# Kernel tuning notes

Hardware: AMD Instinct MI355X
Metric: run time of the kernel (lower is better)

## Reference

```python
import jax, jax.numpy as jnp
import numpy as np

B, D, C = 256, 512, 100000
U_M, L_M = 0.8, 0.45
U_A, L_A = 110.0, 10.0
LAMBDA_G = 35.0
SCALE = 64.0


def setup_inputs() -> dict:
    key = jax.random.key(0)
    k1, k2, k3, k4 = jax.random.split(key, 4)
    x = jax.random.normal(k1, (B, D), dtype=jnp.float32)
    # per-sample feature magnitudes in [l_a, u_a]
    x_norm = L_A + jax.random.uniform(k2, (B, 1), dtype=jnp.float32) * (U_A - L_A)
    labels = jax.random.randint(k3, (B,), 0, C)
    weight = jax.random.normal(k4, (C, D), dtype=jnp.float32)
    return {"x": x, "x_norm": x_norm, "labels": labels, "weight": weight}


def reference(x, x_norm, labels, weight):
    # adaptive margin m(a) = slope * (a - l_a) + l_m, per sample [B,1]
    ada_margin = (U_M - L_M) / (U_A - L_A) * (x_norm - L_A) + L_M
    cos_m = jnp.cos(ada_margin)
    sin_m = jnp.sin(ada_margin)

    xn = x / jnp.linalg.norm(x, axis=-1, keepdims=True)          # [B,D]
    wn = weight / jnp.linalg.norm(weight, axis=-1, keepdims=True)  # [C,D]
    cos_theta = jnp.clip(jnp.einsum('bd,cd->bc', xn, wn), -1.0, 1.0)  # [B,C]
    sin_theta = jnp.sqrt(1.0 - cos_theta * cos_theta)
    cos_theta_m = cos_theta * cos_m - sin_theta * sin_m
    # easy_margin=True: only apply margin where cos_theta > 0
    cos_theta_m = jnp.where(cos_theta > 0, cos_theta_m, cos_theta)

    one_hot = jax.nn.one_hot(labels, C, dtype=cos_theta.dtype)   # [B,C]
    logits = SCALE * (one_hot * cos_theta_m + (1.0 - one_hot) * cos_theta)

    # cross-entropy with mean reduction
    tgt = jnp.take_along_axis(logits, labels[:, None], axis=1)[:, 0]
    ce = jnp.mean(jax.nn.logsumexp(logits, axis=1) - tgt)

    # MagFace G-loss: mean(a / u_a^2 + 1/a)
    loss_g = jnp.mean(x_norm / (U_A * U_A) + 1.0 / x_norm)
    return ce + LAMBDA_G * loss_g
```

## Files before the change

### kernel.cpp

```cpp
#include <hip/hip_runtime.h>
#include <hip/hip_bf16.h>

#define BB 256
#define DD 512
#define CNUM 100000
#define CPAD 100096
#define BN2 64
#define NCH 1564
#define NPART NCH

typedef __attribute__((ext_vector_type(8))) short bf16x8;
typedef __attribute__((ext_vector_type(4))) float f32x4;

__device__ __forceinline__ unsigned short f2bf(float f) {
  union { float f; unsigned int u; } v; v.f = f;
  unsigned int u = v.u;
  unsigned int r = u + 0x7FFFu + ((u >> 16) & 1u);
  return (unsigned short)(r >> 16);
}

__global__ void k_prep_x(const float* __restrict__ x, const float* __restrict__ xnrm,
                         unsigned short* __restrict__ xt, float* __restrict__ cm,
                         float* __restrict__ sm) {
  int b = blockIdx.x;
  int lane = threadIdx.x;
  const float4* xr = (const float4*)(x + (size_t)b * DD);
  float4 v0 = xr[lane * 2];
  float4 v1 = xr[lane * 2 + 1];
  float ss = v0.x * v0.x + v0.y * v0.y + v0.z * v0.z + v0.w * v0.w +
             v1.x * v1.x + v1.y * v1.y + v1.z * v1.z + v1.w * v1.w;
#pragma unroll
  for (int msk = 1; msk < 64; msk <<= 1) ss += __shfl_xor(ss, msk, 64);
  float inv = rsqrtf(ss);
  unsigned int p0 = (unsigned int)f2bf(v0.x * inv) | ((unsigned int)f2bf(v0.y * inv) << 16);
  unsigned int p1 = (unsigned int)f2bf(v0.z * inv) | ((unsigned int)f2bf(v0.w * inv) << 16);
  unsigned int p2 = (unsigned int)f2bf(v1.x * inv) | ((unsigned int)f2bf(v1.y * inv) << 16);
  unsigned int p3 = (unsigned int)f2bf(v1.z * inv) | ((unsigned int)f2bf(v1.w * inv) << 16);
  size_t idx = ((size_t)(lane >> 2) * BB + b) * 32 + (lane & 3) * 8;
  *(uint4*)(xt + idx) = make_uint4(p0, p1, p2, p3);
  if (lane == 0) {
    float a = xnrm[b];
    float marg = 0.0035f * (a - 10.0f) + 0.45f;
    cm[b] = cosf(marg);
    sm[b] = sinf(marg);
  }
}

__global__ __launch_bounds__(256) void k_gemm(
    const unsigned short* __restrict__ xt, const float* __restrict__ w,
    const int* __restrict__ labels, const float* __restrict__ cmv,
    const float* __restrict__ smv, float2* __restrict__ part, float* __restrict__ tgt) {
  __shared__ short Ws[2][BN2 * 64];
  __shared__ float sInvW[BN2];
  __shared__ int sLab[BB];
  __shared__ float sCm[BB], sSm[BB];

  int tid = threadIdx.x, wave = tid >> 6, lane = tid & 63;
  int cbase = blockIdx.x * BN2;
  int cfrag = lane & 15, g = lane >> 4;

  sLab[tid] = labels[tid];
  sCm[tid] = cmv[tid];
  sSm[tid] = smv[tid];

  int wrow = tid >> 2, wseg = tid & 3;
  int wr_c = cbase + wrow;
  if (wr_c >= CNUM) wr_c = 0;
  const float* wptr = w + (size_t)wr_c * DD + wseg * 16;
  float ssacc = 0.0f;
  int wsw0 = wrow * 64 + ((wseg * 16) ^ ((wrow & 7) << 3));
  int wsw1 = wrow * 64 + ((wseg * 16 + 8) ^ ((wrow & 7) << 3));

  const unsigned short* xb = xt + (size_t)(wave * 64 + cfrag) * 32 + g * 8;

  f32x4 acc[4][4];
#pragma unroll
  for (int m = 0; m < 4; ++m)
#pragma unroll
    for (int n = 0; n < 4; ++n) acc[m][n] = (f32x4){0.f, 0.f, 0.f, 0.f};

  f32x4 wv[4];

#define LOAD_W(T)                                                              \
  _Pragma("unroll") for (int j = 0; j < 4; ++j)                                \
      wv[j] = *(const f32x4*)(wptr + (T) * 64 + j * 4);

#define PACK_W(B)                                                              \
  {                                                                            \
    f32x4 a = wv[0], b = wv[1], c = wv[2], d = wv[3];                          \
    ssacc += a[0]*a[0] + a[1]*a[1] + a[2]*a[2] + a[3]*a[3] +                   \
             b[0]*b[0] + b[1]*b[1] + b[2]*b[2] + b[3]*b[3] +                   \
             c[0]*c[0] + c[1]*c[1] + c[2]*c[2] + c[3]*c[3] +                   \
             d[0]*d[0] + d[1]*d[1] + d[2]*d[2] + d[3]*d[3];                    \
    unsigned int q0 = (unsigned int)f2bf(a[0]) | ((unsigned int)f2bf(a[1]) << 16); \
    unsigned int q1 = (unsigned int)f2bf(a[2]) | ((unsigned int)f2bf(a[3]) << 16); \
    unsigned int q2 = (unsigned int)f2bf(b[0]) | ((unsigned int)f2bf(b[1]) << 16); \
    unsigned int q3 = (unsigned int)f2bf(b[2]) | ((unsigned int)f2bf(b[3]) << 16); \
    unsigned int q4 = (unsigned int)f2bf(c[0]) | ((unsigned int)f2bf(c[1]) << 16); \
    unsigned int q5 = (unsigned int)f2bf(c[2]) | ((unsigned int)f2bf(c[3]) << 16); \
    unsigned int q6 = (unsigned int)f2bf(d[0]) | ((unsigned int)f2bf(d[1]) << 16); \
    unsigned int q7 = (unsigned int)f2bf(d[2]) | ((unsigned int)f2bf(d[3]) << 16); \
    *(uint4*)&Ws[B][wsw0] = make_uint4(q0, q1, q2, q3);                        \
    *(uint4*)&Ws[B][wsw1] = make_uint4(q4, q5, q6, q7);                        \
  }

  LOAD_W(0);
  PACK_W(0);
  LOAD_W(1);
  __syncthreads();

#pragma unroll
  for (int kc = 0; kc < 8; ++kc) {
    const int p = kc & 1;
    bf16x8 af0[4], af1[4];
#pragma unroll
    for (int m = 0; m < 4; ++m) {
      af0[m] = *(const bf16x8*)(xb + ((size_t)(2 * kc) * BB + m * 16) * 32);
      af1[m] = *(const bf16x8*)(xb + ((size_t)(2 * kc + 1) * BB + m * 16) * 32);
    }
    if (kc < 7) {
      PACK_W(p ^ 1);
      if (kc < 6) LOAD_W(kc + 2);
    }
#pragma unroll
    for (int ks = 0; ks < 2; ++ks) {
      int krd = ks * 32 + g * 8;
      int swz = (lane & 7) << 3;
      bf16x8 bfr[4];
#pragma unroll
      for (int n = 0; n < 4; ++n) {
        int rb = n * 16 + cfrag;
        bfr[n] = *(const bf16x8*)&Ws[p][rb * 64 + (krd ^ swz)];
      }
#pragma unroll
      for (int m = 0; m < 4; ++m)
#pragma unroll
        for (int n = 0; n < 4; ++n)
          acc[m][n] = __builtin_amdgcn_mfma_f32_16x16x32_bf16(
              ks ? af1[m] : af0[m], bfr[n], acc[m][n], 0, 0, 0);
    }
    __syncthreads();
  }
#undef LOAD_W
#undef PACK_W

  ssacc += __shfl_xor(ssacc, 1, 64);
  ssacc += __shfl_xor(ssacc, 2, 64);
  if (wseg == 0) sInvW[wrow] = rsqrtf(ssacc);
  __syncthreads();

  float invc[4];
#pragma unroll
  for (int n = 0; n < 4; ++n) {
    int col = cbase + n * 16 + cfrag;
    invc[n] = (col < CNUM) ? sInvW[n * 16 + cfrag] : 0.0f;
  }
#pragma unroll
  for (int m = 0; m < 4; ++m) {
#pragma unroll
    for (int r = 0; r < 4; ++r) {
      int row = wave * 64 + m * 16 + g * 4 + r;
      int lab = sLab[row];
      float cmr = sCm[row], smr = sSm[row];
      float lg[4];
      float vmax = -1e30f;
#pragma unroll
      for (int n = 0; n < 4; ++n) {
        int col = cbase + n * 16 + cfrag;
        float cv = acc[m][n][r] * invc[n];
        cv = fminf(1.0f, fmaxf(-1.0f, cv));
        float logit;
        if (col == lab) {
          float st = sqrtf(fmaxf(0.0f, 1.0f - cv * cv));
          float cm2 = cv * cmr - st * smr;
          logit = 64.0f * (cv > 0.0f ? cm2 : cv);
          tgt[row] = logit;
        } else {
          logit = 64.0f * cv;
        }
        if (col >= CNUM) logit = -1e30f;
        lg[n] = logit;
        vmax = fmaxf(vmax, logit);
      }
#pragma unroll
      for (int msk = 1; msk < 16; msk <<= 1) vmax = fmaxf(vmax, __shfl_xor(vmax, msk, 64));
      float s = 0.0f;
#pragma unroll
      for (int n = 0; n < 4; ++n) s += __expf(lg[n] - vmax);
#pragma unroll
      for (int msk = 1; msk < 16; msk <<= 1) s += __shfl_xor(s, msk, 64);
      if (cfrag == 0) part[(size_t)row * NPART + blockIdx.x] = make_float2(vmax, s);
    }
  }
}

__global__ void k_merge(const float2* __restrict__ part, const float* __restrict__ tgt,
                        float* __restrict__ ce) {
  int b = blockIdx.x, t = threadIdx.x;
  float m = -1e30f, s = 0.0f;
  for (int i = t; i < NPART; i += 256) {
    float2 p = part[(size_t)b * NPART + i];
    float nm = fmaxf(m, p.x);
    s = s * __expf(m - nm) + p.y * __expf(p.x - nm);
    m = nm;
  }
  __shared__ float smx[256], ssm[256];
  smx[t] = m;
  ssm[t] = s;
  __syncthreads();
  for (int off = 128; off > 0; off >>= 1) {
    if (t < off) {
      float m2 = smx[t + off], s2 = ssm[t + off];
      float nm = fmaxf(smx[t], m2);
      ssm[t] = ssm[t] * __expf(smx[t] - nm) + s2 * __expf(m2 - nm);
      smx[t] = nm;
    }
    __syncthreads();
  }
  if (t == 0) ce[b] = smx[0] + logf(ssm[0]) - tgt[b];
}

__global__ void k_final(const float* __restrict__ ce, const float* __restrict__ xnrm,
                        float* __restrict__ out) {
  int t = threadIdx.x;
  float cv = ce[t];
  float a = xnrm[t];
  float gv = a * (1.0f / (110.0f * 110.0f)) + 1.0f / a;
  __shared__ float s1[256], s2[256];
  s1[t] = cv;
  s2[t] = gv;
  __syncthreads();
  for (int off = 128; off > 0; off >>= 1) {
    if (t < off) {
      s1[t] += s1[t + off];
      s2[t] += s2[t + off];
    }
    __syncthreads();
  }
  if (t == 0) out[0] = s1[0] * (1.0f / 256.0f) + 35.0f * s2[0] * (1.0f / 256.0f);
}

extern "C" void kernel_launch(void* const* d_in, const int* in_sizes, int n_in,
                              void* d_out, int out_size, void* d_ws, size_t ws_size,
                              hipStream_t stream) {
  const float* x = (const float*)d_in[0];
  const float* xnrm = (const float*)d_in[1];
  const int* labels = (const int*)d_in[2];
  const float* w = (const float*)d_in[3];

  char* ws = (char*)d_ws;
  unsigned short* XT = (unsigned short*)ws;
  size_t off = (size_t)BB * DD * 2;
  float* CM = (float*)(ws + off);  off += 1024;
  float* SM = (float*)(ws + off);  off += 1024;
  float* TGT = (float*)(ws + off); off += 1024;
  float* CE = (float*)(ws + off);  off += 1024;
  float2* PART = (float2*)(ws + off);

  k_prep_x<<<BB, 64, 0, stream>>>(x, xnrm, XT, CM, SM);
  k_gemm<<<NCH, 256, 0, stream>>>(XT, w, labels, CM, SM, PART, TGT);
  k_merge<<<BB, 256, 0, stream>>>(PART, TGT, CE);
  k_final<<<1, 256, 0, stream>>>(CE, xnrm, (float*)d_out);
}
```

Before: 97.47 us.

## Widen GEMM tile to 128 classes per block with 8 waves and register-prefetched A fragments

Each block now covers 128 weight rows with 512 threads arranged as a 4x2 wave grid, halving the grid size while keeping the per-wave 64x64 tile. X fragments are double-buffered in registers and loaded one step ahead. The __syncthreads calls are replaced by lgkmcnt waits plus s_barrier, with compiler fences around the weight loads. The aim is to reuse the X tile across more classes per block and overlap global loads with MFMA work, at the cost of more registers per thread and lower occupancy.

```diff
diff --git a/kernel.cpp b/kernel.cpp
--- a/kernel.cpp
+++ b/kernel.cpp
@@ -5,9 +5,8 @@
 #define DD 512
 #define CNUM 100000
 #define CPAD 100096
-#define BN2 64
-#define NCH 1564
-#define NPART NCH
+#define NCHUNK 782
+#define NPART (NCHUNK * 2)
 
 typedef __attribute__((ext_vector_type(8))) short bf16x8;
 typedef __attribute__((ext_vector_type(4))) float f32x4;
@@ -46,22 +45,25 @@
   }
 }
 
-__global__ __launch_bounds__(256) void k_gemm(
+__global__ __launch_bounds__(512) void k_gemm(
     const unsigned short* __restrict__ xt, const float* __restrict__ w,
     const int* __restrict__ labels, const float* __restrict__ cmv,
     const float* __restrict__ smv, float2* __restrict__ part, float* __restrict__ tgt) {
-  __shared__ short Ws[2][BN2 * 64];
-  __shared__ float sInvW[BN2];
+  __shared__ short Ws[2][128 * 64];
+  __shared__ float sInvW[128];
   __shared__ int sLab[BB];
   __shared__ float sCm[BB], sSm[BB];
 
   int tid = threadIdx.x, wave = tid >> 6, lane = tid & 63;
-  int cbase = blockIdx.x * BN2;
+  int wm = wave >> 1, wq = wave & 1;
+  int cbase = blockIdx.x * 128;
   int cfrag = lane & 15, g = lane >> 4;
 
-  sLab[tid] = labels[tid];
-  sCm[tid] = cmv[tid];
-  sSm[tid] = smv[tid];
+  if (tid < BB) {
+    sLab[tid] = labels[tid];
+    sCm[tid] = cmv[tid];
+    sSm[tid] = smv[tid];
+  }
 
   int wrow = tid >> 2, wseg = tid & 3;
   int wr_c = cbase + wrow;
@@ -71,7 +73,7 @@
   int wsw0 = wrow * 64 + ((wseg * 16) ^ ((wrow & 7) << 3));
   int wsw1 = wrow * 64 + ((wseg * 16 + 8) ^ ((wrow & 7) << 3));
 
-  const unsigned short* xb = xt + (size_t)(wave * 64 + cfrag) * 32 + g * 8;
+  const unsigned short* xtb = xt + (size_t)(wm * 64 + cfrag) * 32 + g * 8;
 
   f32x4 acc[4][4];
 #pragma unroll
@@ -79,15 +81,21 @@
 #pragma unroll
     for (int n = 0; n < 4; ++n) acc[m][n] = (f32x4){0.f, 0.f, 0.f, 0.f};
 
-  f32x4 wv[4];
-
-#define LOAD_W(T)                                                              \
+  f32x4 wv[2][4];
+  bf16x8 af[2][2][4];
+
+#define LOAD_W(T, S)                                                           \
   _Pragma("unroll") for (int j = 0; j < 4; ++j)                                \
-      wv[j] = *(const f32x4*)(wptr + (T) * 64 + j * 4);
-
-#define PACK_W(B)                                                              \
+      wv[S][j] = *(const f32x4*)(wptr + (T) * 64 + j * 4);
+
+#define LOAD_AF(T, S)                                                          \
+  _Pragma("unroll") for (int h = 0; h < 2; ++h)                                \
+  _Pragma("unroll") for (int m = 0; m < 4; ++m)                                \
+      af[S][h][m] = *(const bf16x8*)(xtb + (size_t)(2 * (T) + h) * (BB * 32) + m * 512);
+
+#define PACK_W(S, B)                                                           \
   {                                                                            \
-    f32x4 a = wv[0], b = wv[1], c = wv[2], d = wv[3];                          \
+    f32x4 a = wv[S][0], b = wv[S][1], c = wv[S][2], d = wv[S][3];              \
     ssacc += a[0]*a[0] + a[1]*a[1] + a[2]*a[2] + a[3]*a[3] +                   \
              b[0]*b[0] + b[1]*b[1] + b[2]*b[2] + b[3]*b[3] +                   \
              c[0]*c[0] + c[1]*c[1] + c[2]*c[2] + c[3]*c[3] +                   \
@@ -104,69 +112,72 @@
     *(uint4*)&Ws[B][wsw1] = make_uint4(q4, q5, q6, q7);                        \
   }
 
-  LOAD_W(0);
-  PACK_W(0);
-  LOAD_W(1);
-  __syncthreads();
+#define COMPUTE(T)                                                             \
+  _Pragma("unroll") for (int ks = 0; ks < 2; ++ks) {                           \
+    int krd = ks * 32 + g * 8;                                                 \
+    int swz = (lane & 7) << 3;                                                 \
+    bf16x8 bfr[4];                                                             \
+    _Pragma("unroll") for (int n = 0; n < 4; ++n) {                            \
+      int rb = wq * 64 + n * 16 + cfrag;                                       \
+      bfr[n] = *(const bf16x8*)&Ws[(T) & 1][rb * 64 + (krd ^ swz)];            \
+    }                                                                          \
+    _Pragma("unroll") for (int m = 0; m < 4; ++m)                              \
+      _Pragma("unroll") for (int n = 0; n < 4; ++n)                            \
+        acc[m][n] = __builtin_amdgcn_mfma_f32_16x16x32_bf16(                   \
+            af[(T) & 1][ks][m], bfr[n], acc[m][n], 0, 0, 0);                   \
+  }
+
+#define FENCE asm volatile("" ::: "memory")
+#define BARRIER asm volatile("s_waitcnt lgkmcnt(0)\n\ts_barrier" ::: "memory")
+
+  LOAD_W(0, 0);
+  LOAD_W(1, 1);
+  FENCE;
+  PACK_W(0, 0);
+  LOAD_AF(0, 0);
+  BARRIER;
 
 #pragma unroll
   for (int kc = 0; kc < 8; ++kc) {
-    const int p = kc & 1;
-    bf16x8 af0[4], af1[4];
-#pragma unroll
-    for (int m = 0; m < 4; ++m) {
-      af0[m] = *(const bf16x8*)(xb + ((size_t)(2 * kc) * BB + m * 16) * 32);
-      af1[m] = *(const bf16x8*)(xb + ((size_t)(2 * kc + 1) * BB + m * 16) * 32);
-    }
+    if (kc < 6) { LOAD_W(kc + 2, kc & 1); FENCE; }
+    COMPUTE(kc);
     if (kc < 7) {
-      PACK_W(p ^ 1);
-      if (kc < 6) LOAD_W(kc + 2);
-    }
-#pragma unroll
-    for (int ks = 0; ks < 2; ++ks) {
-      int krd = ks * 32 + g * 8;
-      int swz = (lane & 7) << 3;
-      bf16x8 bfr[4];
-#pragma unroll
-      for (int n = 0; n < 4; ++n) {
-        int rb = n * 16 + cfrag;
-        bfr[n] = *(const bf16x8*)&Ws[p][rb * 64 + (krd ^ swz)];
-      }
-#pragma unroll
-      for (int m = 0; m < 4; ++m)
-#pragma unroll
-        for (int n = 0; n < 4; ++n)
-          acc[m][n] = __builtin_amdgcn_mfma_f32_16x16x32_bf16(
-              ks ? af1[m] : af0[m], bfr[n], acc[m][n], 0, 0, 0);
-    }
-    __syncthreads();
+      PACK_W((kc + 1) & 1, (kc + 1) & 1);
+      LOAD_AF(kc + 1, (kc + 1) & 1);
+      BARRIER;
+    }
   }
 #undef LOAD_W
+#undef LOAD_AF
 #undef PACK_W
+#undef COMPUTE
+#undef FENCE
+#undef BARRIER
 
   ssacc += __shfl_xor(ssacc, 1, 64);
   ssacc += __shfl_xor(ssacc, 2, 64);
+  __syncthreads();
   if (wseg == 0) sInvW[wrow] = rsqrtf(ssacc);
   __syncthreads();
 
   float invc[4];
 #pragma unroll
   for (int n = 0; n < 4; ++n) {
-    int col = cbase + n * 16 + cfrag;
-    invc[n] = (col < CNUM) ? sInvW[n * 16 + cfrag] : 0.0f;
+    int col = cbase + wq * 64 + n * 16 + cfrag;
+    invc[n] = (col < CNUM) ? sInvW[wq * 64 + n * 16 + cfrag] : 0.0f;
   }
 #pragma unroll
   for (int m = 0; m < 4; ++m) {
 #pragma unroll
     for (int r = 0; r < 4; ++r) {
-      int row = wave * 64 + m * 16 + g * 4 + r;
+      int row = wm * 64 + m * 16 + g * 4 + r;
       int lab = sLab[row];
       float cmr = sCm[row], smr = sSm[row];
       float lg[4];
       float vmax = -1e30f;
 #pragma unroll
       for (int n = 0; n < 4; ++n) {
-        int col = cbase + n * 16 + cfrag;
+        int col = cbase + wq * 64 + n * 16 + cfrag;
         float cv = acc[m][n][r] * invc[n];
         cv = fminf(1.0f, fmaxf(-1.0f, cv));
         float logit;
@@ -189,7 +200,7 @@
       for (int n = 0; n < 4; ++n) s += __expf(lg[n] - vmax);
 #pragma unroll
       for (int msk = 1; msk < 16; msk <<= 1) s += __shfl_xor(s, msk, 64);
-      if (cfrag == 0) part[(size_t)row * NPART + blockIdx.x] = make_float2(vmax, s);
+      if (cfrag == 0) part[(size_t)row * NPART + blockIdx.x * 2 + wq] = make_float2(vmax, s);
     }
   }
 }
@@ -258,7 +269,7 @@
   float2* PART = (float2*)(ws + off);
 
   k_prep_x<<<BB, 64, 0, stream>>>(x, xnrm, XT, CM, SM);
-  k_gemm<<<NCH, 256, 0, stream>>>(XT, w, labels, CM, SM, PART, TGT);
+  k_gemm<<<NCHUNK, 512, 0, stream>>>(XT, w, labels, CM, SM, PART, TGT);
   k_merge<<<BB, 256, 0, stream>>>(PART, TGT, CE);
   k_final<<<1, 256, 0, stream>>>(CE, xnrm, (float*)d_out);
 }
```

Result: slower. 101.8 us (+4.5%).
